# Kernel optimization log

Hardware: AMD Instinct MI355X
Metric: run time of the kernel (lower is better)

The kernel has to match this reference:

```python
import jax, jax.numpy as jnp
import numpy as np
from jax import lax

B, P, NB, NF, NC, R = 128, 2048, 2000, 250, 16, 128
LS = NB - NF  # number of simulated bins = len_bins_gensig - 1


def setup_inputs() -> dict:
    key = jax.random.key(0)
    ks = jax.random.split(key, 10)
    return {
        'batched_stim_spat': jax.random.normal(ks[0], (B, P), jnp.float32),
        'stim_time': jax.random.normal(ks[1], (NB,), jnp.float32),
        'batched_initial_spike_section': (jax.random.uniform(ks[2], (B, NF)) < 0.05).astype(jnp.float32),
        'batched_coupling_cells': (jax.random.uniform(ks[3], (B, NC, NB)) < 0.05).astype(jnp.float32),
        'spatial_filter': jax.random.normal(ks[4], (P,), jnp.float32) * 0.02,
        'spatial_bias': jnp.float32(-2.0),
        'stim_timecourse_filter': jax.random.normal(ks[5], (NF,), jnp.float32) * 0.1,
        'feedback_filter': jax.random.normal(ks[6], (NF,), jnp.float32) * 0.05 - 0.02,
        'coupling_filter': jax.random.normal(ks[7], (NC, NF), jnp.float32) * 0.05,
        'u': jax.random.uniform(ks[8], (LS, B, R), jnp.float32),
        'n_repeats': R,
    }


def _corr1d_valid(x, k):
    # torch F.conv1d is cross-correlation; lax conv is too (no kernel flip)
    # x: (n,), k: (m,) -> (n - m + 1,)
    out = lax.conv_general_dilated(x[None, None, :], k[None, None, :], (1,), 'VALID',
                                   dimension_numbers=('NCH', 'OIH', 'NCH'))
    return out[0, 0]


def reference(batched_stim_spat, stim_time, batched_initial_spike_section,
              batched_coupling_cells, spatial_filter, spatial_bias,
              stim_timecourse_filter, feedback_filter, coupling_filter, u, n_repeats):
    nf = stim_timecourse_filter.shape[0]

    # stimulus time component: (n_bins - nf + 1,)
    filt_time = _corr1d_valid(stim_time, stim_timecourse_filter)

    # spatial exp arg for separable linear-spatial GLM:
    # einsum('bpt,p->bt', stim_spat[:,:,None]*filt_time, spatial_filter)
    # factors into outer product of (stim_spat @ spatial_filter) and filt_time
    stim_gensig = (batched_stim_spat @ spatial_filter)[:, None] * filt_time[None, :] + spatial_bias  # (B, T)

    # coupling exp arg: conv1d over all coupled cells -> (B, T)
    coup = lax.conv_general_dilated(batched_coupling_cells, coupling_filter[None, :, :], (1,), 'VALID',
                                    dimension_numbers=('NCH', 'OIH', 'NCH'))[:, 0, :]

    gensig_piece = stim_gensig + coup  # (B, T) with T = n_bins - nf + 1
    len_sim = gensig_piece.shape[1] - 1

    # initial feedback window: last nf spike bins, broadcast over repeats
    batch = batched_stim_spat.shape[0]
    w0 = jnp.broadcast_to(batched_initial_spike_section[:, None, :], (batch, n_repeats, nf)) + 0.0

    def step(window, xs):
        g_t, u_t = xs  # (B,), (B, R)
        fb = jnp.einsum('brk,k->br', window, feedback_filter)
        g = g_t[:, None] + fb
        spike = (u_t < jax.nn.sigmoid(g)).astype(window.dtype)  # Bernoulli(sigmoid(g))
        window = jnp.concatenate([window[:, :, 1:], spike[:, :, None]], axis=2)
        return window, spike

    xs = (jnp.swapaxes(gensig_piece[:, :len_sim], 0, 1), u[:len_sim])  # ((LS,B), (LS,B,R))
    _, spikes = lax.scan(step, w0, xs)  # spikes: (LS, B, R)

    out = jnp.concatenate([w0, jnp.moveaxis(spikes, 0, 2)], axis=2)  # (B, R, n_bins)
    return out
```

## Files before the change

kernel.cpp:

```cpp
#include <hip/hip_runtime.h>
#include <math.h>

#define B_  128
#define P_  2048
#define NB_ 2000
#define NF_ 250
#define NC_ 16
#define R_  128
#define LS_ 1750
#define NT_ 1751
#define BR_ (B_ * R_)
#define H_  16

typedef int v4i __attribute__((ext_vector_type(4)));

template <int CTRL>
__device__ __forceinline__ double dpp64(double v) {
    long long x = __double_as_longlong(v);
    int lo = (int)x, hi = (int)(x >> 32);
    lo = __builtin_amdgcn_mov_dpp(lo, CTRL, 0xF, 0xF, true);
    hi = __builtin_amdgcn_mov_dpp(hi, CTRL, 0xF, 0xF, true);
    return __longlong_as_double(((long long)(unsigned)lo) | ((long long)hi << 32));
}

__device__ __forceinline__ double lu_of(float uf) {
    double u = (double)uf;
    return log(u / (1.0 - u));
}

__global__ __launch_bounds__(256) void k_pre(const float* __restrict__ st,
                                             const float* __restrict__ stf,
                                             const float* __restrict__ sp,
                                             const float* __restrict__ sf,
                                             double* __restrict__ ft,
                                             double* __restrict__ sdot) {
    if (blockIdx.x < 7) {
        int t = blockIdx.x * 256 + threadIdx.x;
        if (t >= NT_) return;
        double s = 0.0;
        for (int k = 0; k < NF_; ++k) s += (double)st[t + k] * (double)stf[k];
        ft[t] = s;
    } else {
        __shared__ double red[256];
        int b = blockIdx.x - 7;
        double s = 0.0;
        for (int p = threadIdx.x; p < P_; p += 256)
            s += (double)sp[(size_t)b * P_ + p] * (double)sf[p];
        red[threadIdx.x] = s;
        __syncthreads();
        for (int off = 128; off > 0; off >>= 1) {
            if (threadIdx.x < off) red[threadIdx.x] += red[threadIdx.x + off];
            __syncthreads();
        }
        if (threadIdx.x == 0) sdot[b] = red[0];
    }
}

__global__ __launch_bounds__(256) void k_coup(const float* __restrict__ cc,
                                              const float* __restrict__ cf,
                                              const double* __restrict__ sdot,
                                              const double* __restrict__ ft,
                                              const float* __restrict__ bias,
                                              double* __restrict__ gensig) {
    __shared__ __align__(16) float  ccs[NC_ * 512];
    __shared__ __align__(16) double cfs[NC_ * 256];
    __shared__ double red[3][64][4];
    int b = blockIdx.y, t0 = blockIdx.x * 256;
    int tid = threadIdx.x, lane = tid & 63, wv = tid >> 6;

    for (int idx = tid; idx < NC_ * 128; idx += 256) {
        int c = idx >> 7, j4 = (idx & 127) * 4, src = t0 + j4;
        const float* p = cc + ((size_t)b * NC_ + c) * NB_ + src;
        float4 v;
        if (src + 3 < NB_) v = *(const float4*)p;
        else {
            v.x = (src     < NB_) ? p[0] : 0.f;
            v.y = (src + 1 < NB_) ? p[1] : 0.f;
            v.z = (src + 2 < NB_) ? p[2] : 0.f;
            v.w = (src + 3 < NB_) ? p[3] : 0.f;
        }
        *(float4*)&ccs[c * 512 + j4] = v;
    }
    for (int idx = tid; idx < NC_ * 256; idx += 256) {
        int c = idx >> 8, k = idx & 255;
        cfs[idx] = (k < NF_) ? (double)cf[c * NF_ + k] : 0.0;
    }
    __syncthreads();

    double a0 = 0, a1 = 0, a2 = 0, a3 = 0;
    int base = lane * 4;
    for (int c = wv; c < NC_; c += 4) {
        const float*  row  = &ccs[c * 512];
        const double* crow = &cfs[c * 256];
        float4 cur = *(const float4*)&row[base];
        for (int k4 = 0; k4 < 252; k4 += 4) {
            float4 nxt = *(const float4*)&row[base + k4 + 4];
            double e0 = cur.x, e1 = cur.y, e2 = cur.z, e3 = cur.w;
            double e4 = nxt.x, e5 = nxt.y, e6 = nxt.z;
            double c0 = crow[k4], c1 = crow[k4 + 1], c2 = crow[k4 + 2], c3 = crow[k4 + 3];
            a0 += e0 * c0 + e1 * c1 + e2 * c2 + e3 * c3;
            a1 += e1 * c0 + e2 * c1 + e3 * c2 + e4 * c3;
            a2 += e2 * c0 + e3 * c1 + e4 * c2 + e5 * c3;
            a3 += e3 * c0 + e4 * c1 + e5 * c2 + e6 * c3;
            cur = nxt;
        }
    }
    if (wv > 0) {
        red[wv - 1][lane][0] = a0; red[wv - 1][lane][1] = a1;
        red[wv - 1][lane][2] = a2; red[wv - 1][lane][3] = a3;
    }
    __syncthreads();
    if (wv == 0) {
        a0 += red[0][lane][0] + red[1][lane][0] + red[2][lane][0];
        a1 += red[0][lane][1] + red[1][lane][1] + red[2][lane][1];
        a2 += red[0][lane][2] + red[1][lane][2] + red[2][lane][2];
        a3 += red[0][lane][3] + red[1][lane][3] + red[2][lane][3];
        double gb = (double)bias[0];
        double sd = sdot[b];
        double accs[4] = {a0, a1, a2, a3};
        int tb = t0 + base;
        for (int i = 0; i < 4; ++i) {
            int t = tb + i;
            if (t < LS_) gensig[(size_t)b * LS_ + t] = sd * ft[t] + gb + accs[i];
        }
    }
}

__global__ __launch_bounds__(256, 1) void k_scan(const double* __restrict__ gensig,
                                                 const float* __restrict__ u,
                                                 const float* __restrict__ iss,
                                                 const float* __restrict__ ff,
                                                 float* __restrict__ out) {
    __shared__ double   farT_all[4][16 * 17];
    __shared__ unsigned q2_all[4][16];
    int tid = threadIdx.x;
    int wv = tid >> 6, l = tid & 63;
    int gw = blockIdx.x * 4 + wv;
    int b = gw >> 3, rbase = (gw & 7) * 16;
    double*   farT = &farT_all[wv][0];
    unsigned* q2s  = &q2_all[wv][0];

    int lw = l & 15;
    int q  = l >> 4;
    int cn = l >> 2;
    int j  = l & 3;

    const float* issb = iss + b * NF_;
    for (int idx = l; idx < 16 * NF_; idx += 64) {
        int c = idx / NF_, k = idx - c * NF_;
        out[((size_t)(b * R_ + rbase + c)) * NB_ + k] = issb[k];
    }

    unsigned long long W[4] = {0ull, 0ull, 0ull, 0ull};
    for (int k = 0; k < NF_; ++k) {
        unsigned long long bit = (issb[k] > 0.5f) ? 1ull : 0ull;
        W[k >> 6] |= bit << (k & 63);
    }

    int Bword[4][7][4];
#pragma unroll
    for (int kc = 0; kc < 4; ++kc)
#pragma unroll
        for (int p = 0; p < 7; ++p)
#pragma unroll
            for (int w = 0; w < 4; ++w) Bword[kc][p][w] = 0;
#pragma unroll
    for (int kc = 0; kc < 4; ++kc) {
#pragma unroll
        for (int jj = 0; jj < 16; ++jj) {
            int k = kc * 64 + q * 16 + jj;
            int idx = k - lw;
            long long v = 0;
            if (idx >= 0 && idx < NF_)
                v = __double2ll_rn((double)ff[idx] * 281474976710656.0);
#pragma unroll
            for (int p = 0; p < 7; ++p) {
                int d = (int)((v + 128) & 255) - 128;
                v = (v - (long long)d) >> 8;
                Bword[kc][p][jj >> 2] |= (d & 255) << ((jj & 3) * 8);
            }
        }
    }
    v4i Bf[4][7];
#pragma unroll
    for (int kc = 0; kc < 4; ++kc)
#pragma unroll
        for (int p = 0; p < 7; ++p) {
            v4i t; t.x = Bword[kc][p][0]; t.y = Bword[kc][p][1];
            t.z = Bword[kc][p][2]; t.w = Bword[kc][p][3];
            Bf[kc][p] = t;
        }

    const double* gs = gensig + (size_t)b * LS_;
    const float*  up = u + b * R_ + rbase + cn;
    float*        op = out + ((size_t)(b * R_ + rbase + cn)) * NB_ + NF_;

    double tp0 = (double)ff[249 - 4 * j];
    double tp1 = (double)ff[248 - 4 * j];
    double tp2 = (double)ff[247 - 4 * j];
    double tp3 = (double)ff[246 - 4 * j];

    double farv[16];
    double mylu0 = 0, mylu1 = 0, mylu2 = 0, mylu3 = 0;
    float  uraw0, uraw1, uraw2, uraw3;
    double gprep = gs[lw];
    {
        int t_;
        t_ = 0  + j; if (t_ > LS_ - 1) t_ = LS_ - 1; uraw0 = up[(size_t)t_ * BR_];
        t_ = 4  + j; if (t_ > LS_ - 1) t_ = LS_ - 1; uraw1 = up[(size_t)t_ * BR_];
        t_ = 8  + j; if (t_ > LS_ - 1) t_ = LS_ - 1; uraw2 = up[(size_t)t_ * BR_];
        t_ = 12 + j; if (t_ > LS_ - 1) t_ = LS_ - 1; uraw3 = up[(size_t)t_ * BR_];
    }

#define NSTEP(i, S, MYLU) { \
    double lu = dpp64<(S) * 0x55>(MYLU); \
    unsigned qb = qreg >> (4 * j); \
    double n0 = (qb & 1u) ? tp0 : 0.0; \
    double n1 = (qb & 2u) ? tp1 : 0.0; \
    double n2 = (qb & 4u) ? tp2 : 0.0; \
    double n3 = (qb & 8u) ? tp3 : 0.0; \
    double ns = (n0 + n1) + (n2 + n3); \
    ns += dpp64<0xB1>(ns); \
    ns += dpp64<0x4E>(ns); \
    bool sp = (farv[i] + ns) > lu; \
    qreg = (qreg << 1) | (sp ? 1u : 0u); \
}

    for (int t0 = -H_; t0 < LS_; t0 += H_) {
        if (t0 >= 0) {
            unsigned qreg = 0;
            NSTEP(0,  0, mylu0) NSTEP(1,  1, mylu0) NSTEP(2,  2, mylu0) NSTEP(3,  3, mylu0)
            NSTEP(4,  0, mylu1) NSTEP(5,  1, mylu1) NSTEP(6,  2, mylu1) NSTEP(7,  3, mylu1)
            NSTEP(8,  0, mylu2) NSTEP(9,  1, mylu2) NSTEP(10, 2, mylu2) NSTEP(11, 3, mylu2)
            NSTEP(12, 0, mylu3) NSTEP(13, 1, mylu3) NSTEP(14, 2, mylu3) NSTEP(15, 3, mylu3)

            unsigned q2 = __brev(qreg) >> 16;
            int rem = LS_ - t0; if (rem > H_) rem = H_;
            int s0 = 4 * j;
            if (s0 + 3 < rem) {
                float4 o;
                o.x = (float)((q2 >> (s0    )) & 1u);
                o.y = (float)((q2 >> (s0 + 1)) & 1u);
                o.z = (float)((q2 >> (s0 + 2)) & 1u);
                o.w = (float)((q2 >> (s0 + 3)) & 1u);
                *(float4*)(op + t0 + s0) = o;
            } else {
#pragma unroll
                for (int e = 0; e < 4; ++e)
                    if (s0 + e < rem) op[t0 + s0 + e] = (float)((q2 >> (s0 + e)) & 1u);
            }
            if (j == 0) q2s[cn] = q2;
            __asm__ volatile("s_waitcnt lgkmcnt(0)" ::: "memory");
            unsigned long long q2n = (unsigned long long)q2s[lw];
            W[0] = (W[0] >> 16) | (W[1] << 48);
            W[1] = (W[1] >> 16) | (W[2] << 48);
            W[2] = (W[2] >> 16) | (W[3] << 48);
            W[3] = (W[3] >> 16) | (q2n << 42);
        }

        int P = t0 + H_;
        if (P < LS_) {
            v4i acc[7];
#pragma unroll
            for (int p = 0; p < 7; ++p) acc[p] = (v4i){0, 0, 0, 0};
#pragma unroll
            for (int kc = 0; kc < 4; ++kc) {
                unsigned field = (unsigned)((W[kc] >> (q * 16)) & 0xFFFFull);
                v4i av;
                av.x = (int)((((field      ) & 0xFu) * 0x00204081u) & 0x01010101u);
                av.y = (int)((((field >>  4) & 0xFu) * 0x00204081u) & 0x01010101u);
                av.z = (int)((((field >>  8) & 0xFu) * 0x00204081u) & 0x01010101u);
                av.w = (int)((((field >> 12) & 0xFu) * 0x00204081u) & 0x01010101u);
#pragma unroll
                for (int p = 0; p < 7; ++p)
                    acc[p] = __builtin_amdgcn_mfma_i32_16x16x64_i8(av, Bf[kc][p], acc[p], 0, 0, 0);
            }
#pragma unroll
            for (int r = 0; r < 4; ++r) {
                double fb = gprep;
#pragma unroll
                for (int p = 0; p < 7; ++p)
                    fb += (double)acc[p][r] * ldexp(1.0, 8 * p - 48);
                farT[(q * 4 + r) * 17 + lw] = fb;
            }
            __asm__ volatile("s_waitcnt lgkmcnt(0)" ::: "memory");
#pragma unroll
            for (int i = 0; i < 16; ++i) farv[i] = farT[cn * 17 + i];

            {
                int tg = P + H_ + lw; if (tg > LS_ - 1) tg = LS_ - 1;
                gprep = gs[tg];
            }
            mylu0 = lu_of(uraw0); mylu1 = lu_of(uraw1);
            mylu2 = lu_of(uraw2); mylu3 = lu_of(uraw3);
            {
                int t_;
                t_ = P + H_ +  0 + j; if (t_ > LS_ - 1) t_ = LS_ - 1; uraw0 = up[(size_t)t_ * BR_];
                t_ = P + H_ +  4 + j; if (t_ > LS_ - 1) t_ = LS_ - 1; uraw1 = up[(size_t)t_ * BR_];
                t_ = P + H_ +  8 + j; if (t_ > LS_ - 1) t_ = LS_ - 1; uraw2 = up[(size_t)t_ * BR_];
                t_ = P + H_ + 12 + j; if (t_ > LS_ - 1) t_ = LS_ - 1; uraw3 = up[(size_t)t_ * BR_];
            }
        }
    }
#undef NSTEP
}

extern "C" void kernel_launch(void* const* d_in, const int* in_sizes, int n_in,
                              void* d_out, int out_size, void* d_ws, size_t ws_size,
                              hipStream_t stream) {
    const float* stim_spat = (const float*)d_in[0];
    const float* stim_time = (const float*)d_in[1];
    const float* iss       = (const float*)d_in[2];
    const float* cc        = (const float*)d_in[3];
    const float* sf        = (const float*)d_in[4];
    const float* bias      = (const float*)d_in[5];
    const float* stf       = (const float*)d_in[6];
    const float* ff        = (const float*)d_in[7];
    const float* cf        = (const float*)d_in[8];
    const float* u         = (const float*)d_in[9];
    (void)in_sizes; (void)n_in; (void)out_size; (void)ws_size;

    float* out = (float*)d_out;

    double* ws     = (double*)d_ws;
    double* gensig = ws;
    double* ft     = gensig + (size_t)B_ * LS_;
    double* sdot   = ft + NT_;

    k_pre  <<<135, 256, 0, stream>>>(stim_time, stf, stim_spat, sf, ft, sdot);
    k_coup <<<dim3(7, B_), 256, 0, stream>>>(cc, cf, sdot, ft, bias, gensig);
    k_scan <<<B_ * 2, 256, 0, stream>>>(gensig, u, iss, ff, out);
}
```

Before: 589.3 us.

## Widen exact near-window, cut MFMA passes, precompute logit of u, reorder scan pipeline

```diff
diff --git a/kernel.cpp b/kernel.cpp
--- a/kernel.cpp
+++ b/kernel.cpp
@@ -126,19 +126,30 @@
     }
 }
 
+__global__ __launch_bounds__(256) void k_lu(const float* __restrict__ u,
+                                            double* __restrict__ lu) {
+    size_t i = ((size_t)blockIdx.x * 256 + (size_t)threadIdx.x) * 4;
+    float4 v = *(const float4*)(u + i);
+    double2 o0, o1;
+    o0.x = lu_of(v.x); o0.y = lu_of(v.y);
+    o1.x = lu_of(v.z); o1.y = lu_of(v.w);
+    *(double2*)(lu + i)     = o0;
+    *(double2*)(lu + i + 2) = o1;
+}
+
+template <int PRE>
 __global__ __launch_bounds__(256, 1) void k_scan(const double* __restrict__ gensig,
                                                  const float* __restrict__ u,
+                                                 const double* __restrict__ luws,
                                                  const float* __restrict__ iss,
                                                  const float* __restrict__ ff,
                                                  float* __restrict__ out) {
-    __shared__ double   farT_all[4][16 * 17];
-    __shared__ unsigned q2_all[4][16];
+    __shared__ double farT_all[4][16 * 17];
     int tid = threadIdx.x;
     int wv = tid >> 6, l = tid & 63;
     int gw = blockIdx.x * 4 + wv;
     int b = gw >> 3, rbase = (gw & 7) * 16;
-    double*   farT = &farT_all[wv][0];
-    unsigned* q2s  = &q2_all[wv][0];
+    double* farT = &farT_all[wv][0];
 
     int lw = l & 15;
     int q  = l >> 4;
@@ -151,17 +162,20 @@
         out[((size_t)(b * R_ + rbase + c)) * NB_ + k] = issb[k];
     }
 
-    unsigned long long W[4] = {0ull, 0ull, 0ull, 0ull};
+    unsigned long long W0 = 0, W1 = 0, W2 = 0, W3 = 0;
     for (int k = 0; k < NF_; ++k) {
         unsigned long long bit = (issb[k] > 0.5f) ? 1ull : 0ull;
-        W[k >> 6] |= bit << (k & 63);
-    }
-
-    int Bword[4][7][4];
+        if      (k <  64) W0 |= bit << k;
+        else if (k < 128) W1 |= bit << (k - 64);
+        else if (k < 192) W2 |= bit << (k - 128);
+        else              W3 |= bit << (k - 192);
+    }
+
+    int Bword[4][5][4];
 #pragma unroll
     for (int kc = 0; kc < 4; ++kc)
 #pragma unroll
-        for (int p = 0; p < 7; ++p)
+        for (int p = 0; p < 5; ++p)
 #pragma unroll
             for (int w = 0; w < 4; ++w) Bword[kc][p][w] = 0;
 #pragma unroll
@@ -171,134 +185,172 @@
             int k = kc * 64 + q * 16 + jj;
             int idx = k - lw;
             long long v = 0;
-            if (idx >= 0 && idx < NF_)
-                v = __double2ll_rn((double)ff[idx] * 281474976710656.0);
-#pragma unroll
-            for (int p = 0; p < 7; ++p) {
+            if (idx >= 0 && idx <= 217)
+                v = __double2ll_rn((double)ff[idx] * 1099511627776.0);
+#pragma unroll
+            for (int p = 0; p < 5; ++p) {
                 int d = (int)((v + 128) & 255) - 128;
                 v = (v - (long long)d) >> 8;
                 Bword[kc][p][jj >> 2] |= (d & 255) << ((jj & 3) * 8);
             }
         }
     }
-    v4i Bf[4][7];
+    v4i Bf[4][5];
 #pragma unroll
     for (int kc = 0; kc < 4; ++kc)
 #pragma unroll
-        for (int p = 0; p < 7; ++p) {
+        for (int p = 0; p < 5; ++p) {
             v4i t; t.x = Bword[kc][p][0]; t.y = Bword[kc][p][1];
             t.z = Bword[kc][p][2]; t.w = Bword[kc][p][3];
             Bf[kc][p] = t;
         }
 
-    const double* gs = gensig + (size_t)b * LS_;
-    const float*  up = u + b * R_ + rbase + cn;
-    float*        op = out + ((size_t)(b * R_ + rbase + cn)) * NB_ + NF_;
-
-    double tp0 = (double)ff[249 - 4 * j];
-    double tp1 = (double)ff[248 - 4 * j];
-    double tp2 = (double)ff[247 - 4 * j];
-    double tp3 = (double)ff[246 - 4 * j];
-
+    const double* gs  = gensig + (size_t)b * LS_;
+    const float*  up  = u    + b * R_ + rbase + cn;
+    const double* lup = luws + b * R_ + rbase + cn;
+    float*        op  = out + ((size_t)(b * R_ + rbase + cn)) * NB_ + NF_;
+
+    double tp0 = (double)ff[249 - 8 * j];
+    double tp1 = (double)ff[248 - 8 * j];
+    double tp2 = (double)ff[247 - 8 * j];
+    double tp3 = (double)ff[246 - 8 * j];
+    double tp4 = (double)ff[245 - 8 * j];
+    double tp5 = (double)ff[244 - 8 * j];
+    double tp6 = (double)ff[243 - 8 * j];
+    double tp7 = (double)ff[242 - 8 * j];
+
+    unsigned qreg = __brev((unsigned)(W3 >> 26));
+
+    auto do_far = [&](unsigned long long S0, unsigned long long S1,
+                      unsigned long long S2, unsigned long long S3, double gp) {
+        unsigned long long Sarr[4] = {S0, S1, S2, S3};
+        v4i acc[5];
+#pragma unroll
+        for (int p = 0; p < 5; ++p) acc[p] = (v4i){0, 0, 0, 0};
+#pragma unroll
+        for (int kc = 0; kc < 4; ++kc) {
+            unsigned f = (unsigned)((Sarr[kc] >> (q * 16)) & 0xFFFFull);
+            v4i av;
+            av.x = (int)((((f      ) & 0xFu) * 0x00204081u) & 0x01010101u);
+            av.y = (int)((((f >>  4) & 0xFu) * 0x00204081u) & 0x01010101u);
+            av.z = (int)((((f >>  8) & 0xFu) * 0x00204081u) & 0x01010101u);
+            av.w = (int)((((f >> 12) & 0xFu) * 0x00204081u) & 0x01010101u);
+#pragma unroll
+            for (int p = 0; p < 5; ++p)
+                acc[p] = __builtin_amdgcn_mfma_i32_16x16x64_i8(av, Bf[kc][p], acc[p], 0, 0, 0);
+        }
+#pragma unroll
+        for (int r = 0; r < 4; ++r) {
+            int lo = acc[0][r] + 256 * acc[1][r] + 65536 * acc[2][r];
+            int hi = acc[3][r] + 256 * acc[4][r];
+            double fb = gp + (double)lo * 0x1p-40 + (double)hi * 0x1p-16;
+            farT[(q * 4 + r) * 17 + lw] = fb;
+        }
+    };
+
+    do_far(W0, W1, W2, W3, gs[lw]);
+    __asm__ volatile("s_waitcnt lgkmcnt(0)" ::: "memory");
     double farv[16];
-    double mylu0 = 0, mylu1 = 0, mylu2 = 0, mylu3 = 0;
-    float  uraw0, uraw1, uraw2, uraw3;
-    double gprep = gs[lw];
+#pragma unroll
+    for (int i = 0; i < 16; ++i) farv[i] = farT[cn * 17 + i];
+
+    double gprep;
+    { int tg = 16 + lw; if (tg > LS_ - 1) tg = LS_ - 1; gprep = gs[tg]; }
+
+    double mylu0, mylu1, mylu2, mylu3;
+    double nlu0 = 0, nlu1 = 0, nlu2 = 0, nlu3 = 0;
+    float  ur0 = 0, ur1 = 0, ur2 = 0, ur3 = 0;
     {
         int t_;
-        t_ = 0  + j; if (t_ > LS_ - 1) t_ = LS_ - 1; uraw0 = up[(size_t)t_ * BR_];
-        t_ = 4  + j; if (t_ > LS_ - 1) t_ = LS_ - 1; uraw1 = up[(size_t)t_ * BR_];
-        t_ = 8  + j; if (t_ > LS_ - 1) t_ = LS_ - 1; uraw2 = up[(size_t)t_ * BR_];
-        t_ = 12 + j; if (t_ > LS_ - 1) t_ = LS_ - 1; uraw3 = up[(size_t)t_ * BR_];
+        if (PRE) {
+            t_ = 0  + j; mylu0 = lup[(size_t)t_ * BR_];
+            t_ = 4  + j; mylu1 = lup[(size_t)t_ * BR_];
+            t_ = 8  + j; mylu2 = lup[(size_t)t_ * BR_];
+            t_ = 12 + j; mylu3 = lup[(size_t)t_ * BR_];
+            t_ = 16 + j; nlu0 = lup[(size_t)t_ * BR_];
+            t_ = 20 + j; nlu1 = lup[(size_t)t_ * BR_];
+            t_ = 24 + j; nlu2 = lup[(size_t)t_ * BR_];
+            t_ = 28 + j; nlu3 = lup[(size_t)t_ * BR_];
+        } else {
+            t_ = 0  + j; mylu0 = lu_of(up[(size_t)t_ * BR_]);
+            t_ = 4  + j; mylu1 = lu_of(up[(size_t)t_ * BR_]);
+            t_ = 8  + j; mylu2 = lu_of(up[(size_t)t_ * BR_]);
+            t_ = 12 + j; mylu3 = lu_of(up[(size_t)t_ * BR_]);
+            t_ = 16 + j; ur0 = up[(size_t)t_ * BR_];
+            t_ = 20 + j; ur1 = up[(size_t)t_ * BR_];
+            t_ = 24 + j; ur2 = up[(size_t)t_ * BR_];
+            t_ = 28 + j; ur3 = up[(size_t)t_ * BR_];
+        }
     }
 
 #define NSTEP(i, S, MYLU) { \
     double lu = dpp64<(S) * 0x55>(MYLU); \
-    unsigned qb = qreg >> (4 * j); \
-    double n0 = (qb & 1u) ? tp0 : 0.0; \
-    double n1 = (qb & 2u) ? tp1 : 0.0; \
-    double n2 = (qb & 4u) ? tp2 : 0.0; \
-    double n3 = (qb & 8u) ? tp3 : 0.0; \
-    double ns = (n0 + n1) + (n2 + n3); \
-    ns += dpp64<0xB1>(ns); \
-    ns += dpp64<0x4E>(ns); \
-    bool sp = (farv[i] + ns) > lu; \
+    unsigned qb = (qreg >> (8 * j)) & 255u; \
+    double s = ((((qb & 1u)  ? tp0 : 0.0) + ((qb & 2u)  ? tp1 : 0.0)) + \
+                (((qb & 4u)  ? tp2 : 0.0) + ((qb & 8u)  ? tp3 : 0.0))) + \
+               ((((qb & 16u) ? tp4 : 0.0) + ((qb & 32u) ? tp5 : 0.0)) + \
+                (((qb & 64u) ? tp6 : 0.0) + ((qb & 128u)? tp7 : 0.0))); \
+    s += dpp64<0xB1>(s); \
+    s += dpp64<0x4E>(s); \
+    bool sp = (farv[i] + s) > lu; \
     qreg = (qreg << 1) | (sp ? 1u : 0u); \
 }
 
-    for (int t0 = -H_; t0 < LS_; t0 += H_) {
-        if (t0 >= 0) {
-            unsigned qreg = 0;
-            NSTEP(0,  0, mylu0) NSTEP(1,  1, mylu0) NSTEP(2,  2, mylu0) NSTEP(3,  3, mylu0)
-            NSTEP(4,  0, mylu1) NSTEP(5,  1, mylu1) NSTEP(6,  2, mylu1) NSTEP(7,  3, mylu1)
-            NSTEP(8,  0, mylu2) NSTEP(9,  1, mylu2) NSTEP(10, 2, mylu2) NSTEP(11, 3, mylu2)
-            NSTEP(12, 0, mylu3) NSTEP(13, 1, mylu3) NSTEP(14, 2, mylu3) NSTEP(15, 3, mylu3)
-
-            unsigned q2 = __brev(qreg) >> 16;
-            int rem = LS_ - t0; if (rem > H_) rem = H_;
-            int s0 = 4 * j;
-            if (s0 + 3 < rem) {
-                float4 o;
-                o.x = (float)((q2 >> (s0    )) & 1u);
-                o.y = (float)((q2 >> (s0 + 1)) & 1u);
-                o.z = (float)((q2 >> (s0 + 2)) & 1u);
-                o.w = (float)((q2 >> (s0 + 3)) & 1u);
-                *(float4*)(op + t0 + s0) = o;
+    for (int t0 = 0; t0 < LS_; t0 += H_) {
+        bool more = (t0 + H_ < LS_);
+        if (more) {
+            do_far((W0 >> 16) | (W1 << 48), (W1 >> 16) | (W2 << 48),
+                   (W2 >> 16) | (W3 << 48), (W3 >> 16), gprep);
+            int tg = t0 + 32 + lw; if (tg > LS_ - 1) tg = LS_ - 1;
+            gprep = gs[tg];
+        }
+
+        NSTEP(0,  0, mylu0) NSTEP(1,  1, mylu0) NSTEP(2,  2, mylu0) NSTEP(3,  3, mylu0)
+        NSTEP(4,  0, mylu1) NSTEP(5,  1, mylu1) NSTEP(6,  2, mylu1) NSTEP(7,  3, mylu1)
+        NSTEP(8,  0, mylu2) NSTEP(9,  1, mylu2) NSTEP(10, 2, mylu2) NSTEP(11, 3, mylu2)
+        NSTEP(12, 0, mylu3) NSTEP(13, 1, mylu3) NSTEP(14, 2, mylu3) NSTEP(15, 3, mylu3)
+
+        unsigned q2 = (__brev(qreg) >> 16) & 0xFFFFu;
+        int rem = LS_ - t0; if (rem > H_) rem = H_;
+        int s0 = 4 * j;
+        if (s0 + 3 < rem) {
+            float4 o;
+            o.x = (float)((q2 >> (s0    )) & 1u);
+            o.y = (float)((q2 >> (s0 + 1)) & 1u);
+            o.z = (float)((q2 >> (s0 + 2)) & 1u);
+            o.w = (float)((q2 >> (s0 + 3)) & 1u);
+            *(float4*)(op + t0 + s0) = o;
+        } else {
+#pragma unroll
+            for (int e = 0; e < 4; ++e)
+                if (s0 + e < rem) op[t0 + s0 + e] = (float)((q2 >> (s0 + e)) & 1u);
+        }
+
+        if (more) {
+            int q2i = __builtin_amdgcn_ds_bpermute(lw << 4, (int)q2);
+            unsigned long long q2n = (unsigned long long)(unsigned)q2i;
+            W0 = (W0 >> 16) | (W1 << 48);
+            W1 = (W1 >> 16) | (W2 << 48);
+            W2 = (W2 >> 16) | (W3 << 48);
+            W3 = (W3 >> 16) | (q2n << 42);
+            __asm__ volatile("s_waitcnt lgkmcnt(0)" ::: "memory");
+#pragma unroll
+            for (int i = 0; i < 16; ++i) farv[i] = farT[cn * 17 + i];
+
+            int t_;
+            if (PRE) {
+                mylu0 = nlu0; mylu1 = nlu1; mylu2 = nlu2; mylu3 = nlu3;
+                t_ = t0 + 32 +  0 + j; if (t_ > LS_ - 1) t_ = LS_ - 1; nlu0 = lup[(size_t)t_ * BR_];
+                t_ = t0 + 32 +  4 + j; if (t_ > LS_ - 1) t_ = LS_ - 1; nlu1 = lup[(size_t)t_ * BR_];
+                t_ = t0 + 32 +  8 + j; if (t_ > LS_ - 1) t_ = LS_ - 1; nlu2 = lup[(size_t)t_ * BR_];
+                t_ = t0 + 32 + 12 + j; if (t_ > LS_ - 1) t_ = LS_ - 1; nlu3 = lup[(size_t)t_ * BR_];
             } else {
-#pragma unroll
-                for (int e = 0; e < 4; ++e)
-                    if (s0 + e < rem) op[t0 + s0 + e] = (float)((q2 >> (s0 + e)) & 1u);
-            }
-            if (j == 0) q2s[cn] = q2;
-            __asm__ volatile("s_waitcnt lgkmcnt(0)" ::: "memory");
-            unsigned long long q2n = (unsigned long long)q2s[lw];
-            W[0] = (W[0] >> 16) | (W[1] << 48);
-            W[1] = (W[1] >> 16) | (W[2] << 48);
-            W[2] = (W[2] >> 16) | (W[3] << 48);
-            W[3] = (W[3] >> 16) | (q2n << 42);
-        }
-
-        int P = t0 + H_;
-        if (P < LS_) {
-            v4i acc[7];
-#pragma unroll
-            for (int p = 0; p < 7; ++p) acc[p] = (v4i){0, 0, 0, 0};
-#pragma unroll
-            for (int kc = 0; kc < 4; ++kc) {
-                unsigned field = (unsigned)((W[kc] >> (q * 16)) & 0xFFFFull);
-                v4i av;
-                av.x = (int)((((field      ) & 0xFu) * 0x00204081u) & 0x01010101u);
-                av.y = (int)((((field >>  4) & 0xFu) * 0x00204081u) & 0x01010101u);
-                av.z = (int)((((field >>  8) & 0xFu) * 0x00204081u) & 0x01010101u);
-                av.w = (int)((((field >> 12) & 0xFu) * 0x00204081u) & 0x01010101u);
-#pragma unroll
-                for (int p = 0; p < 7; ++p)
-                    acc[p] = __builtin_amdgcn_mfma_i32_16x16x64_i8(av, Bf[kc][p], acc[p], 0, 0, 0);
-            }
-#pragma unroll
-            for (int r = 0; r < 4; ++r) {
-                double fb = gprep;
-#pragma unroll
-                for (int p = 0; p < 7; ++p)
-                    fb += (double)acc[p][r] * ldexp(1.0, 8 * p - 48);
-                farT[(q * 4 + r) * 17 + lw] = fb;
-            }
-            __asm__ volatile("s_waitcnt lgkmcnt(0)" ::: "memory");
-#pragma unroll
-            for (int i = 0; i < 16; ++i) farv[i] = farT[cn * 17 + i];
-
-            {
-                int tg = P + H_ + lw; if (tg > LS_ - 1) tg = LS_ - 1;
-                gprep = gs[tg];
-            }
-            mylu0 = lu_of(uraw0); mylu1 = lu_of(uraw1);
-            mylu2 = lu_of(uraw2); mylu3 = lu_of(uraw3);
-            {
-                int t_;
-                t_ = P + H_ +  0 + j; if (t_ > LS_ - 1) t_ = LS_ - 1; uraw0 = up[(size_t)t_ * BR_];
-                t_ = P + H_ +  4 + j; if (t_ > LS_ - 1) t_ = LS_ - 1; uraw1 = up[(size_t)t_ * BR_];
-                t_ = P + H_ +  8 + j; if (t_ > LS_ - 1) t_ = LS_ - 1; uraw2 = up[(size_t)t_ * BR_];
-                t_ = P + H_ + 12 + j; if (t_ > LS_ - 1) t_ = LS_ - 1; uraw3 = up[(size_t)t_ * BR_];
+                mylu0 = lu_of(ur0); mylu1 = lu_of(ur1);
+                mylu2 = lu_of(ur2); mylu3 = lu_of(ur3);
+                t_ = t0 + 32 +  0 + j; if (t_ > LS_ - 1) t_ = LS_ - 1; ur0 = up[(size_t)t_ * BR_];
+                t_ = t0 + 32 +  4 + j; if (t_ > LS_ - 1) t_ = LS_ - 1; ur1 = up[(size_t)t_ * BR_];
+                t_ = t0 + 32 +  8 + j; if (t_ > LS_ - 1) t_ = LS_ - 1; ur2 = up[(size_t)t_ * BR_];
+                t_ = t0 + 32 + 12 + j; if (t_ > LS_ - 1) t_ = LS_ - 1; ur3 = up[(size_t)t_ * BR_];
             }
         }
     }
@@ -318,7 +370,7 @@
     const float* ff        = (const float*)d_in[7];
     const float* cf        = (const float*)d_in[8];
     const float* u         = (const float*)d_in[9];
-    (void)in_sizes; (void)n_in; (void)out_size; (void)ws_size;
+    (void)in_sizes; (void)n_in; (void)out_size;
 
     float* out = (float*)d_out;
 
@@ -326,8 +378,17 @@
     double* gensig = ws;
     double* ft     = gensig + (size_t)B_ * LS_;
     double* sdot   = ft + NT_;
+    const size_t lu_off = 225880;
+    double* lu_ws  = ws + lu_off;
+    size_t need = (lu_off + (size_t)LS_ * BR_) * sizeof(double);
+    bool pre = (ws_size >= need);
 
     k_pre  <<<135, 256, 0, stream>>>(stim_time, stf, stim_spat, sf, ft, sdot);
     k_coup <<<dim3(7, B_), 256, 0, stream>>>(cc, cf, sdot, ft, bias, gensig);
-    k_scan <<<B_ * 2, 256, 0, stream>>>(gensig, u, iss, ff, out);
-}
+    if (pre) {
+        k_lu   <<<(LS_ * BR_) / 1024, 256, 0, stream>>>(u, lu_ws);
+        k_scan<1><<<B_ * 2, 256, 0, stream>>>(gensig, u, lu_ws, iss, ff, out);
+    } else {
+        k_scan<0><<<B_ * 2, 256, 0, stream>>>(gensig, u, lu_ws, iss, ff, out);
+    }
+}
```

New measurement: 743.0 us. 26.1% more time.

## Use fixed-point integer thresholds in spike scan and trim MFMA limbs

Applied to the files above, without the earlier changes.

```diff
diff --git a/kernel.cpp b/kernel.cpp
--- a/kernel.cpp
+++ b/kernel.cpp
@@ -15,17 +15,35 @@
 typedef int v4i __attribute__((ext_vector_type(4)));
 
 template <int CTRL>
-__device__ __forceinline__ double dpp64(double v) {
-    long long x = __double_as_longlong(v);
+__device__ __forceinline__ long long dpp64i(long long x) {
     int lo = (int)x, hi = (int)(x >> 32);
     lo = __builtin_amdgcn_mov_dpp(lo, CTRL, 0xF, 0xF, true);
     hi = __builtin_amdgcn_mov_dpp(hi, CTRL, 0xF, 0xF, true);
-    return __longlong_as_double(((long long)(unsigned)lo) | ((long long)hi << 32));
-}
-
-__device__ __forceinline__ double lu_of(float uf) {
+    return ((long long)(unsigned)lo) | ((long long)hi << 32);
+}
+
+__device__ __forceinline__ double logit_fast(float uf) {
     double u = (double)uf;
-    return log(u / (1.0 - u));
+    double v = 1.0 - u;
+    double qd = u / v;
+    long long bits = __double_as_longlong(qd);
+    int e = (int)((bits >> 52) & 0x7FF) - 1023;
+    double m = __longlong_as_double((bits & 0xFFFFFFFFFFFFFLL) | 0x3FF0000000000000LL);
+    if (m > 1.4142135623730951) { m *= 0.5; e += 1; }
+    double s = (m - 1.0) / (m + 1.0);
+    double z = s * s;
+    double Q = fma(z, fma(z, fma(z, fma(z, fma(z, fma(z,
+        0.06666666666666667, 0.07692307692307693), 0.09090909090909091),
+        0.1111111111111111), 0.14285714285714285), 0.2), 0.3333333333333333);
+    double logm = fma(2.0 * s, z * Q, 2.0 * s);
+    return fma((double)e, 0.6931471805599453, logm);
+}
+
+__device__ __forceinline__ long long thrq_of(double lu, double fb) {
+    double thr = lu - fb;
+    thr = fmin(fmax(thr, -8.0), 8.0);
+    double d = fma(thr, 0x1p45, 0x1.8p52);
+    return (__double_as_longlong(d) & 0xFFFFFFFFFFFFFLL) - (1LL << 51);
 }
 
 __global__ __launch_bounds__(256) void k_pre(const float* __restrict__ st,
@@ -131,14 +149,12 @@
                                                  const float* __restrict__ iss,
                                                  const float* __restrict__ ff,
                                                  float* __restrict__ out) {
-    __shared__ double   farT_all[4][16 * 17];
-    __shared__ unsigned q2_all[4][16];
+    __shared__ double farT_all[4][16 * 17];
     int tid = threadIdx.x;
     int wv = tid >> 6, l = tid & 63;
     int gw = blockIdx.x * 4 + wv;
     int b = gw >> 3, rbase = (gw & 7) * 16;
-    double*   farT = &farT_all[wv][0];
-    unsigned* q2s  = &q2_all[wv][0];
+    double* farT = &farT_all[wv][0];
 
     int lw = l & 15;
     int q  = l >> 4;
@@ -151,17 +167,20 @@
         out[((size_t)(b * R_ + rbase + c)) * NB_ + k] = issb[k];
     }
 
-    unsigned long long W[4] = {0ull, 0ull, 0ull, 0ull};
+    unsigned long long W0 = 0, W1 = 0, W2 = 0, W3 = 0;
     for (int k = 0; k < NF_; ++k) {
         unsigned long long bit = (issb[k] > 0.5f) ? 1ull : 0ull;
-        W[k >> 6] |= bit << (k & 63);
-    }
-
-    int Bword[4][7][4];
+        if      (k <  64) W0 |= bit << k;
+        else if (k < 128) W1 |= bit << (k - 64);
+        else if (k < 192) W2 |= bit << (k - 128);
+        else              W3 |= bit << (k - 192);
+    }
+
+    int Bword[4][6][4];
 #pragma unroll
     for (int kc = 0; kc < 4; ++kc)
 #pragma unroll
-        for (int p = 0; p < 7; ++p)
+        for (int p = 0; p < 6; ++p)
 #pragma unroll
             for (int w = 0; w < 4; ++w) Bword[kc][p][w] = 0;
 #pragma unroll
@@ -174,18 +193,18 @@
             if (idx >= 0 && idx < NF_)
                 v = __double2ll_rn((double)ff[idx] * 281474976710656.0);
 #pragma unroll
-            for (int p = 0; p < 7; ++p) {
+            for (int p = 0; p < 6; ++p) {
                 int d = (int)((v + 128) & 255) - 128;
                 v = (v - (long long)d) >> 8;
                 Bword[kc][p][jj >> 2] |= (d & 255) << ((jj & 3) * 8);
             }
         }
     }
-    v4i Bf[4][7];
+    v4i Bf[4][6];
 #pragma unroll
     for (int kc = 0; kc < 4; ++kc)
 #pragma unroll
-        for (int p = 0; p < 7; ++p) {
+        for (int p = 0; p < 6; ++p) {
             v4i t; t.x = Bword[kc][p][0]; t.y = Bword[kc][p][1];
             t.z = Bword[kc][p][2]; t.w = Bword[kc][p][3];
             Bf[kc][p] = t;
@@ -195,111 +214,124 @@
     const float*  up = u + b * R_ + rbase + cn;
     float*        op = out + ((size_t)(b * R_ + rbase + cn)) * NB_ + NF_;
 
-    double tp0 = (double)ff[249 - 4 * j];
-    double tp1 = (double)ff[248 - 4 * j];
-    double tp2 = (double)ff[247 - 4 * j];
-    double tp3 = (double)ff[246 - 4 * j];
-
-    double farv[16];
-    double mylu0 = 0, mylu1 = 0, mylu2 = 0, mylu3 = 0;
-    float  uraw0, uraw1, uraw2, uraw3;
+    long long tq0 = __double2ll_rn((double)ff[249 - 4 * j] * 0x1p45);
+    long long tq1 = __double2ll_rn((double)ff[248 - 4 * j] * 0x1p45);
+    long long tq2 = __double2ll_rn((double)ff[247 - 4 * j] * 0x1p45);
+    long long tq3 = __double2ll_rn((double)ff[246 - 4 * j] * 0x1p45);
+
+    auto do_far = [&](double gp) {
+        unsigned long long Sarr[4] = {W0, W1, W2, W3};
+        v4i acc[6];
+#pragma unroll
+        for (int p = 0; p < 6; ++p) acc[p] = (v4i){0, 0, 0, 0};
+#pragma unroll
+        for (int kc = 0; kc < 4; ++kc) {
+            unsigned f = (unsigned)((Sarr[kc] >> (q * 16)) & 0xFFFFull);
+            v4i av;
+            av.x = (int)((((f      ) & 0xFu) * 0x00204081u) & 0x01010101u);
+            av.y = (int)((((f >>  4) & 0xFu) * 0x00204081u) & 0x01010101u);
+            av.z = (int)((((f >>  8) & 0xFu) * 0x00204081u) & 0x01010101u);
+            av.w = (int)((((f >> 12) & 0xFu) * 0x00204081u) & 0x01010101u);
+#pragma unroll
+            for (int p = 0; p < 6; ++p)
+                acc[p] = __builtin_amdgcn_mfma_i32_16x16x64_i8(av, Bf[kc][p], acc[p], 0, 0, 0);
+        }
+#pragma unroll
+        for (int r = 0; r < 4; ++r) {
+            int lo = acc[0][r] + acc[1][r] * 256 + acc[2][r] * 65536;
+            int hi = acc[3][r] + acc[4][r] * 256 + acc[5][r] * 65536;
+            double fb = gp + (double)lo * 0x1p-48 + (double)hi * 0x1p-24;
+            farT[(q * 4 + r) * 17 + lw] = fb;
+        }
+    };
+
     double gprep = gs[lw];
+    float ur0, ur1, ur2, ur3;
     {
         int t_;
-        t_ = 0  + j; if (t_ > LS_ - 1) t_ = LS_ - 1; uraw0 = up[(size_t)t_ * BR_];
-        t_ = 4  + j; if (t_ > LS_ - 1) t_ = LS_ - 1; uraw1 = up[(size_t)t_ * BR_];
-        t_ = 8  + j; if (t_ > LS_ - 1) t_ = LS_ - 1; uraw2 = up[(size_t)t_ * BR_];
-        t_ = 12 + j; if (t_ > LS_ - 1) t_ = LS_ - 1; uraw3 = up[(size_t)t_ * BR_];
-    }
-
-#define NSTEP(i, S, MYLU) { \
-    double lu = dpp64<(S) * 0x55>(MYLU); \
-    unsigned qb = qreg >> (4 * j); \
-    double n0 = (qb & 1u) ? tp0 : 0.0; \
-    double n1 = (qb & 2u) ? tp1 : 0.0; \
-    double n2 = (qb & 4u) ? tp2 : 0.0; \
-    double n3 = (qb & 8u) ? tp3 : 0.0; \
-    double ns = (n0 + n1) + (n2 + n3); \
-    ns += dpp64<0xB1>(ns); \
-    ns += dpp64<0x4E>(ns); \
-    bool sp = (farv[i] + ns) > lu; \
+        t_ = 0  + j; ur0 = up[(size_t)t_ * BR_];
+        t_ = 4  + j; ur1 = up[(size_t)t_ * BR_];
+        t_ = 8  + j; ur2 = up[(size_t)t_ * BR_];
+        t_ = 12 + j; ur3 = up[(size_t)t_ * BR_];
+    }
+    long long thrq0, thrq1, thrq2, thrq3;
+    do_far(gprep);
+    {
+        double lu0 = logit_fast(ur0), lu1 = logit_fast(ur1);
+        double lu2 = logit_fast(ur2), lu3 = logit_fast(ur3);
+        __asm__ volatile("s_waitcnt lgkmcnt(0)" ::: "memory");
+        thrq0 = thrq_of(lu0, farT[cn * 17 + j]);
+        thrq1 = thrq_of(lu1, farT[cn * 17 + 4 + j]);
+        thrq2 = thrq_of(lu2, farT[cn * 17 + 8 + j]);
+        thrq3 = thrq_of(lu3, farT[cn * 17 + 12 + j]);
+    }
+    { int tg = 16 + lw; if (tg > LS_ - 1) tg = LS_ - 1; gprep = gs[tg]; }
+    {
+        int t_;
+        t_ = 16 + j;      if (t_ > LS_ - 1) t_ = LS_ - 1; ur0 = up[(size_t)t_ * BR_];
+        t_ = 20 + j;      if (t_ > LS_ - 1) t_ = LS_ - 1; ur1 = up[(size_t)t_ * BR_];
+        t_ = 24 + j;      if (t_ > LS_ - 1) t_ = LS_ - 1; ur2 = up[(size_t)t_ * BR_];
+        t_ = 28 + j;      if (t_ > LS_ - 1) t_ = LS_ - 1; ur3 = up[(size_t)t_ * BR_];
+    }
+
+#define NSTEP(S, THRQ) { \
+    long long thr = dpp64i<(S) * 0x55>(THRQ); \
+    unsigned qb = (qreg >> (4 * j)) & 15u; \
+    long long s = (((qb & 1u) ? tq0 : 0LL) + ((qb & 2u) ? tq1 : 0LL)) \
+                + (((qb & 4u) ? tq2 : 0LL) + ((qb & 8u) ? tq3 : 0LL)); \
+    s += dpp64i<0xB1>(s); \
+    s += dpp64i<0x4E>(s); \
+    bool sp = s > thr; \
     qreg = (qreg << 1) | (sp ? 1u : 0u); \
 }
 
-    for (int t0 = -H_; t0 < LS_; t0 += H_) {
-        if (t0 >= 0) {
-            unsigned qreg = 0;
-            NSTEP(0,  0, mylu0) NSTEP(1,  1, mylu0) NSTEP(2,  2, mylu0) NSTEP(3,  3, mylu0)
-            NSTEP(4,  0, mylu1) NSTEP(5,  1, mylu1) NSTEP(6,  2, mylu1) NSTEP(7,  3, mylu1)
-            NSTEP(8,  0, mylu2) NSTEP(9,  1, mylu2) NSTEP(10, 2, mylu2) NSTEP(11, 3, mylu2)
-            NSTEP(12, 0, mylu3) NSTEP(13, 1, mylu3) NSTEP(14, 2, mylu3) NSTEP(15, 3, mylu3)
-
-            unsigned q2 = __brev(qreg) >> 16;
-            int rem = LS_ - t0; if (rem > H_) rem = H_;
-            int s0 = 4 * j;
-            if (s0 + 3 < rem) {
-                float4 o;
-                o.x = (float)((q2 >> (s0    )) & 1u);
-                o.y = (float)((q2 >> (s0 + 1)) & 1u);
-                o.z = (float)((q2 >> (s0 + 2)) & 1u);
-                o.w = (float)((q2 >> (s0 + 3)) & 1u);
-                *(float4*)(op + t0 + s0) = o;
-            } else {
-#pragma unroll
-                for (int e = 0; e < 4; ++e)
-                    if (s0 + e < rem) op[t0 + s0 + e] = (float)((q2 >> (s0 + e)) & 1u);
-            }
-            if (j == 0) q2s[cn] = q2;
+    for (int t0 = 0; t0 < LS_; t0 += H_) {
+        unsigned qreg = 0;
+        NSTEP(0, thrq0) NSTEP(1, thrq0) NSTEP(2, thrq0) NSTEP(3, thrq0)
+        NSTEP(0, thrq1) NSTEP(1, thrq1) NSTEP(2, thrq1) NSTEP(3, thrq1)
+        NSTEP(0, thrq2) NSTEP(1, thrq2) NSTEP(2, thrq2) NSTEP(3, thrq2)
+        NSTEP(0, thrq3) NSTEP(1, thrq3) NSTEP(2, thrq3) NSTEP(3, thrq3)
+
+        unsigned q2 = (__brev(qreg) >> 16) & 0xFFFFu;
+        int rem = LS_ - t0; if (rem > H_) rem = H_;
+        int s0 = 4 * j;
+        if (s0 + 3 < rem) {
+            float4 o;
+            o.x = (float)((q2 >> (s0    )) & 1u);
+            o.y = (float)((q2 >> (s0 + 1)) & 1u);
+            o.z = (float)((q2 >> (s0 + 2)) & 1u);
+            o.w = (float)((q2 >> (s0 + 3)) & 1u);
+            *(float4*)(op + t0 + s0) = o;
+        } else {
+#pragma unroll
+            for (int e = 0; e < 4; ++e)
+                if (s0 + e < rem) op[t0 + s0 + e] = (float)((q2 >> (s0 + e)) & 1u);
+        }
+
+        if (t0 + H_ < LS_) {
+            int q2i = __builtin_amdgcn_ds_bpermute(lw << 4, (int)q2);
+            unsigned long long q2n = (unsigned long long)(unsigned)q2i;
+            W0 = (W0 >> 16) | (W1 << 48);
+            W1 = (W1 >> 16) | (W2 << 48);
+            W2 = (W2 >> 16) | (W3 << 48);
+            W3 = (W3 >> 16) | (q2n << 42);
+
+            do_far(gprep);
+            double lu0 = logit_fast(ur0), lu1 = logit_fast(ur1);
+            double lu2 = logit_fast(ur2), lu3 = logit_fast(ur3);
             __asm__ volatile("s_waitcnt lgkmcnt(0)" ::: "memory");
-            unsigned long long q2n = (unsigned long long)q2s[lw];
-            W[0] = (W[0] >> 16) | (W[1] << 48);
-            W[1] = (W[1] >> 16) | (W[2] << 48);
-            W[2] = (W[2] >> 16) | (W[3] << 48);
-            W[3] = (W[3] >> 16) | (q2n << 42);
-        }
-
-        int P = t0 + H_;
-        if (P < LS_) {
-            v4i acc[7];
-#pragma unroll
-            for (int p = 0; p < 7; ++p) acc[p] = (v4i){0, 0, 0, 0};
-#pragma unroll
-            for (int kc = 0; kc < 4; ++kc) {
-                unsigned field = (unsigned)((W[kc] >> (q * 16)) & 0xFFFFull);
-                v4i av;
-                av.x = (int)((((field      ) & 0xFu) * 0x00204081u) & 0x01010101u);
-                av.y = (int)((((field >>  4) & 0xFu) * 0x00204081u) & 0x01010101u);
-                av.z = (int)((((field >>  8) & 0xFu) * 0x00204081u) & 0x01010101u);
-                av.w = (int)((((field >> 12) & 0xFu) * 0x00204081u) & 0x01010101u);
-#pragma unroll
-                for (int p = 0; p < 7; ++p)
-                    acc[p] = __builtin_amdgcn_mfma_i32_16x16x64_i8(av, Bf[kc][p], acc[p], 0, 0, 0);
-            }
-#pragma unroll
-            for (int r = 0; r < 4; ++r) {
-                double fb = gprep;
-#pragma unroll
-                for (int p = 0; p < 7; ++p)
-                    fb += (double)acc[p][r] * ldexp(1.0, 8 * p - 48);
-                farT[(q * 4 + r) * 17 + lw] = fb;
-            }
-            __asm__ volatile("s_waitcnt lgkmcnt(0)" ::: "memory");
-#pragma unroll
-            for (int i = 0; i < 16; ++i) farv[i] = farT[cn * 17 + i];
-
-            {
-                int tg = P + H_ + lw; if (tg > LS_ - 1) tg = LS_ - 1;
-                gprep = gs[tg];
-            }
-            mylu0 = lu_of(uraw0); mylu1 = lu_of(uraw1);
-            mylu2 = lu_of(uraw2); mylu3 = lu_of(uraw3);
-            {
-                int t_;
-                t_ = P + H_ +  0 + j; if (t_ > LS_ - 1) t_ = LS_ - 1; uraw0 = up[(size_t)t_ * BR_];
-                t_ = P + H_ +  4 + j; if (t_ > LS_ - 1) t_ = LS_ - 1; uraw1 = up[(size_t)t_ * BR_];
-                t_ = P + H_ +  8 + j; if (t_ > LS_ - 1) t_ = LS_ - 1; uraw2 = up[(size_t)t_ * BR_];
-                t_ = P + H_ + 12 + j; if (t_ > LS_ - 1) t_ = LS_ - 1; uraw3 = up[(size_t)t_ * BR_];
-            }
+            thrq0 = thrq_of(lu0, farT[cn * 17 + j]);
+            thrq1 = thrq_of(lu1, farT[cn * 17 + 4 + j]);
+            thrq2 = thrq_of(lu2, farT[cn * 17 + 8 + j]);
+            thrq3 = thrq_of(lu3, farT[cn * 17 + 12 + j]);
+
+            int tg = t0 + 32 + lw; if (tg > LS_ - 1) tg = LS_ - 1;
+            gprep = gs[tg];
+            int t_;
+            t_ = t0 + 32 +  0 + j; if (t_ > LS_ - 1) t_ = LS_ - 1; ur0 = up[(size_t)t_ * BR_];
+            t_ = t0 + 32 +  4 + j; if (t_ > LS_ - 1) t_ = LS_ - 1; ur1 = up[(size_t)t_ * BR_];
+            t_ = t0 + 32 +  8 + j; if (t_ > LS_ - 1) t_ = LS_ - 1; ur2 = up[(size_t)t_ * BR_];
+            t_ = t0 + 32 + 12 + j; if (t_ > LS_ - 1) t_ = LS_ - 1; ur3 = up[(size_t)t_ * BR_];
         }
     }
 #undef NSTEP
```

New measurement: 553.0 us. -6.2%, faster.
